# Performance work log

Hardware: AMD Instinct MI355X
Metric: run time of the kernel (lower is better)

## Reference

```python
import jax, jax.numpy as jnp
import numpy as np

B, C, H, W = 32, 3, 512, 512
OUT = (64, 64)  # (out_grid[0]=Nx, out_grid[1]=Ny)
SMALL = 1e-4


def setup_inputs() -> dict:
    key = jax.random.key(0)
    k1, k2 = jax.random.split(key, 2)
    X = jax.random.normal(k1, (B, C, H, W), dtype=jnp.float32)
    fan_in = C * H * W
    # localization net: flatten + dense(5); scaled so p ~ N(0,1) and exp(p) is stable
    W_loc = jax.random.normal(k2, (fan_in, 5), dtype=jnp.float32) / np.float32(np.sqrt(fan_in))
    b_loc = jnp.zeros((5,), dtype=jnp.float32)
    return {"X": X, "W_loc": W_loc, "b_loc": b_loc}


def reference(X, W_loc, b_loc):
    Bn = X.shape[0]
    # locnet: p = flatten(X) @ W_loc + b_loc  -> [B, 5]
    p = X.reshape(Bn, -1) @ W_loc + b_loc

    N = min(OUT)
    gx = OUT[0] * (p[:, 0] + 1.0) / 2.0          # [B]
    gy = OUT[1] * (p[:, 1] + 1.0) / 2.0          # [B]
    sigma2 = jnp.exp(p[:, 2])                    # [B]
    delta = jnp.exp(p[:, 3]) * (max(W, H) - 1) / (N - 1.0)  # [B]
    gamma = jnp.exp(p[:, 4])                     # [B]

    i1 = jnp.arange(OUT[0], dtype=jnp.float32)   # [Nx]
    i2 = jnp.arange(OUT[1], dtype=jnp.float32)   # [Ny]
    a = jnp.arange(W, dtype=jnp.float32)         # [W]
    b = jnp.arange(H, dtype=jnp.float32)         # [H]

    mx = gx[:, None] + delta[:, None] * (i1 - N / 2.0 - 0.5)  # [B, Nx]
    my = gy[:, None] + delta[:, None] * (i2 - N / 2.0 - 0.5)  # [B, Ny]

    Fx = jnp.exp(-((a - mx[:, :, None]) ** 2) / (2.0 * sigma2[:, None, None]))  # [B,Nx,W]
    Fx = Fx / (Fx.sum(axis=-1, keepdims=True) + SMALL)
    Fy = jnp.exp(-((b - my[:, :, None]) ** 2) / (2.0 * sigma2[:, None, None]))  # [B,Ny,H]
    Fy = Fy / (Fy.sum(axis=-1, keepdims=True) + SMALL)

    # glimpse read: gamma * Fy @ X @ Fx^T, done as batched contractions
    Fyx = jnp.einsum('bnh,bchw->bcnw', Fy, X)        # [B,C,Ny,W]
    out = jnp.einsum('bcnw,bmw->bcnm', Fyx, Fx)      # [B,C,Ny,Nx]
    return gamma[:, None, None, None] * out
```

## Files before the change

kernel.cpp:

```cpp
#include <hip/hip_runtime.h>
#include <math.h>

#define B_ 32
#define C_ 3
#define H_ 512
#define W_ 512
#define NOUT 64
#define FAN (C_*H_*W_)

#define CHUNKS 192
#define CELEMS (FAN / CHUNKS)
#define BGROUPS 4

#define PPART_STRIDE 160
#define GAMMA_OFF (CHUNKS * PPART_STRIDE)
#define PFLOATS 32768
#define FXH_U 0
#define FXL_U 1048576
#define FYH_U 2097152
#define FYL_U 3145728

typedef __bf16 bf16x8 __attribute__((ext_vector_type(8)));
typedef float f32x4 __attribute__((ext_vector_type(4)));

__device__ __forceinline__ unsigned short f2bf(float f) {
    unsigned int u = __float_as_uint(f);
    u = (u + 0x7FFFu + ((u >> 16) & 1u)) >> 16;
    return (unsigned short)u;
}
__device__ __forceinline__ float bf2f(unsigned short h) {
    return __uint_as_float(((unsigned int)h) << 16);
}
__device__ __forceinline__ unsigned int cvt_pk_bf16(float lo, float hi) {
    unsigned int r;
    asm("v_cvt_pk_bf16_f32 %0, %1, %2" : "=v"(r) : "v"(lo), "v"(hi));
    return r;
}

__global__ __launch_bounds__(256) void k_locnet(const float* __restrict__ X,
                                                const float* __restrict__ Wl,
                                                float* __restrict__ ws) {
    const int chunk = blockIdx.x;
    const int b0 = blockIdx.y * 8;
    const int t = threadIdx.x;

    float acc[8][5] = {};
    const size_t base = (size_t)chunk * CELEMS;

    for (int k = t; k < CELEMS / 4; k += 256) {
        const size_t i0 = base + (size_t)k * 4;
        const float4* W4 = (const float4*)(Wl + i0 * 5);
        float4 w0 = W4[0], w1 = W4[1], w2 = W4[2], w3 = W4[3], w4 = W4[4];
        float wv[20] = {w0.x, w0.y, w0.z, w0.w,
                        w1.x, w1.y, w1.z, w1.w,
                        w2.x, w2.y, w2.z, w2.w,
                        w3.x, w3.y, w3.z, w3.w,
                        w4.x, w4.y, w4.z, w4.w};
        #pragma unroll
        for (int bb = 0; bb < 8; bb++) {
            float4 x = *(const float4*)(X + (size_t)(b0 + bb) * FAN + i0);
            float xv[4] = {x.x, x.y, x.z, x.w};
            #pragma unroll
            for (int e = 0; e < 4; e++)
                #pragma unroll
                for (int j = 0; j < 5; j++)
                    acc[bb][j] += xv[e] * wv[e * 5 + j];
        }
    }

    #pragma unroll
    for (int off = 32; off > 0; off >>= 1)
        #pragma unroll
        for (int bb = 0; bb < 8; bb++)
            #pragma unroll
            for (int j = 0; j < 5; j++)
                acc[bb][j] += __shfl_down(acc[bb][j], off);

    __shared__ float sred[4][40];
    const int wave = t >> 6, lane = t & 63;
    if (lane == 0) {
        #pragma unroll
        for (int bb = 0; bb < 8; bb++)
            #pragma unroll
            for (int j = 0; j < 5; j++)
                sred[wave][bb * 5 + j] = acc[bb][j];
    }
    __syncthreads();
    if (t < 40) {
        float s = sred[0][t] + sred[1][t] + sred[2][t] + sred[3][t];
        ws[(size_t)chunk * PPART_STRIDE + b0 * 5 + t] = s;
    }
}

__global__ __launch_bounds__(256) void k_filters(const float* __restrict__ bl,
                                                 float* __restrict__ ws,
                                                 float* __restrict__ out) {
    const int n = blockIdx.x;
    const int b = blockIdx.y;
    const int which = blockIdx.z;
    const int t = threadIdx.x;

    {
        const int bid = blockIdx.x + NOUT * (blockIdx.y + B_ * blockIdx.z);
        if (t < 24) {
            ((float4*)out)[(size_t)bid * 24 + t] = make_float4(0.f, 0.f, 0.f, 0.f);
        }
    }

    float pj[5] = {0.f, 0.f, 0.f, 0.f, 0.f};
    if (t < CHUNKS) {
        const float* pr = ws + (size_t)t * PPART_STRIDE + b * 5;
        #pragma unroll
        for (int j = 0; j < 5; j++) pj[j] = pr[j];
    }
    #pragma unroll
    for (int off = 32; off > 0; off >>= 1)
        #pragma unroll
        for (int j = 0; j < 5; j++) pj[j] += __shfl_down(pj[j], off);

    __shared__ float spart[4][5];
    __shared__ float pfin[5];
    const int wave = t >> 6, lane = t & 63;
    if (lane == 0) {
        #pragma unroll
        for (int j = 0; j < 5; j++) spart[wave][j] = pj[j];
    }
    __syncthreads();
    if (t < 5) pfin[t] = spart[0][t] + spart[1][t] + spart[2][t] + spart[3][t] + bl[t];
    __syncthreads();

    const float p0 = pfin[0], p1 = pfin[1], p2 = pfin[2], p3 = pfin[3];
    if (which == 0 && n == 0 && t == 0) ws[GAMMA_OFF + b] = expf(pfin[4]);

    const float g = (which == 0) ? 32.f * (p0 + 1.f) : 32.f * (p1 + 1.f);
    const float sigma2 = expf(p2);
    const float inv2s = 0.5f / sigma2;
    const float delta = expf(p3) * (511.0f / 63.0f);
    const float mean = g + delta * ((float)n - 32.5f);

    float d0 = (float)(2 * t) - mean;
    float f0 = expf(-d0 * d0 * inv2s);
    float d1 = (float)(2 * t + 1) - mean;
    float f1 = expf(-d1 * d1 * inv2s);

    float s = f0 + f1;
    #pragma unroll
    for (int off = 32; off > 0; off >>= 1) s += __shfl_down(s, off);
    __shared__ float sred[4];
    __shared__ float stot;
    if (lane == 0) sred[wave] = s;
    __syncthreads();
    if (t == 0) stot = sred[0] + sred[1] + sred[2] + sred[3] + 1e-4f;
    __syncthreads();
    const float scale = 1.0f / stot;

    unsigned short* wsu = (unsigned short*)(ws + PFLOATS);
    unsigned int* dstH = (unsigned int*)(wsu + (which ? FYH_U : FXH_U) + ((size_t)b * NOUT + n) * 512);
    unsigned int* dstL = (unsigned int*)(wsu + (which ? FYL_U : FXL_U) + ((size_t)b * NOUT + n) * 512);

    float v0 = f0 * scale;
    float v1 = f1 * scale;
    unsigned short h0 = f2bf(v0);
    unsigned short h1 = f2bf(v1);
    unsigned short l0 = f2bf(v0 - bf2f(h0));
    unsigned short l1 = f2bf(v1 - bf2f(h1));
    dstH[t] = (unsigned int)h0 | ((unsigned int)h1 << 16);
    dstL[t] = (unsigned int)l0 | ((unsigned int)l1 << 16);
}

#define KC 64
#define PITCH 72
#define TSZ (64 * PITCH)

#define LOAD_X(wt_) do {                                                      \
    const int wbase_ = (wt_) * KC;                                            \
    _Pragma("unroll")                                                         \
    for (int k4 = 0; k4 < 4; k4++) {                                          \
        int idx_ = t + 256 * k4;                                              \
        int row_ = idx_ >> 4;                                                 \
        int c4_ = (idx_ & 15) * 4;                                            \
        xr[k4] = *(const float4*)(Xp + (size_t)row_ * W_ + wbase_ + c4_);     \
    } } while (0)

#define LOAD_F(Hp_, Lp_, coff_) do {                                          \
    _Pragma("unroll")                                                         \
    for (int i_ = 0; i_ < 2; i_++) {                                          \
        int idx_ = t + 256 * i_;                                              \
        int row_ = idx_ >> 3;                                                 \
        int c8_ = (idx_ & 7) * 8;                                             \
        fhr[i_] = *(const uint4*)((Hp_) + (size_t)row_ * 512 + (coff_) + c8_);\
        flr[i_] = *(const uint4*)((Lp_) + (size_t)row_ * 512 + (coff_) + c8_);\
    } } while (0)

__global__ __launch_bounds__(256) void k_glimpse(const float* __restrict__ X,
                                                 const float* __restrict__ ws,
                                                 float* __restrict__ out) {
    const int hc = blockIdx.x;
    const int bc = blockIdx.y;
    const int b = bc / 3;
    const int t = threadIdx.x;
    const int lane = t & 63;
    const int wv = t >> 6;
    const int l15 = lane & 15;
    const int quad = lane >> 4;
    const int hbase = hc * 64;

    __shared__ __align__(16) unsigned short lds[4 * TSZ];
    unsigned short* Xh = lds;
    unsigned short* Xl = lds + TSZ;
    unsigned short* Fh = lds + 2 * TSZ;
    unsigned short* Fl = lds + 3 * TSZ;

    const float* Xp = X + (size_t)bc * (H_ * W_) + (size_t)hbase * W_;
    const unsigned short* wsu = (const unsigned short*)(ws + PFLOATS);
    const unsigned short* FxHp = wsu + FXH_U + (size_t)b * NOUT * 512;
    const unsigned short* FxLp = wsu + FXL_U + (size_t)b * NOUT * 512;
    const unsigned short* FyHp = wsu + FYH_U + (size_t)b * NOUT * 512;
    const unsigned short* FyLp = wsu + FYL_U + (size_t)b * NOUT * 512;

    float4 xr[4];
    uint4 fhr[2], flr[2];
    LOAD_X(0);
    LOAD_F(FxHp, FxLp, 0);

    f32x4 acc[4] = {};

    for (int wt = 0; wt < 8; wt++) {
        #pragma unroll
        for (int k4 = 0; k4 < 4; k4++) {
            int idx = t + 256 * k4;
            int row = idx >> 4;
            int c4 = (idx & 15) * 4;
            float4 v = xr[k4];
            unsigned int h01 = cvt_pk_bf16(v.x, v.y);
            unsigned int h23 = cvt_pk_bf16(v.z, v.w);
            float r0 = __uint_as_float(h01 << 16);
            float r1 = __uint_as_float(h01 & 0xffff0000u);
            float r2 = __uint_as_float(h23 << 16);
            float r3 = __uint_as_float(h23 & 0xffff0000u);
            unsigned int l01 = cvt_pk_bf16(v.x - r0, v.y - r1);
            unsigned int l23 = cvt_pk_bf16(v.z - r2, v.w - r3);
            int o = row * PITCH + c4;
            *(uint2*)&Xh[o] = make_uint2(h01, h23);
            *(uint2*)&Xl[o] = make_uint2(l01, l23);
        }
        #pragma unroll
        for (int i = 0; i < 2; i++) {
            int idx = t + 256 * i;
            int row = idx >> 3;
            int c8 = (idx & 7) * 8;
            *(uint4*)&Fh[row * PITCH + c8] = fhr[i];
            *(uint4*)&Fl[row * PITCH + c8] = flr[i];
        }
        __syncthreads();

        if (wt < 7) {
            LOAD_X(wt + 1);
            LOAD_F(FxHp, FxLp, (wt + 1) * KC);
        } else {
            LOAD_F(FyHp, FyLp, hbase);
        }

        #pragma unroll
        for (int ks = 0; ks < 2; ks++) {
            const int ko = ks * 32 + quad * 8;
            bf16x8 ah = *(const bf16x8*)&Xh[(16 * wv + l15) * PITCH + ko];
            bf16x8 al = *(const bf16x8*)&Xl[(16 * wv + l15) * PITCH + ko];
            #pragma unroll
            for (int mt = 0; mt < 4; mt++) {
                bf16x8 bh = *(const bf16x8*)&Fh[(16 * mt + l15) * PITCH + ko];
                bf16x8 bl2 = *(const bf16x8*)&Fl[(16 * mt + l15) * PITCH + ko];
                acc[mt] = __builtin_amdgcn_mfma_f32_16x16x32_bf16(ah, bh, acc[mt], 0, 0, 0);
                acc[mt] = __builtin_amdgcn_mfma_f32_16x16x32_bf16(al, bh, acc[mt], 0, 0, 0);
                acc[mt] = __builtin_amdgcn_mfma_f32_16x16x32_bf16(ah, bl2, acc[mt], 0, 0, 0);
            }
        }
        __syncthreads();
    }

    #pragma unroll
    for (int mt = 0; mt < 4; mt++) {
        float g0 = acc[mt][0], g1 = acc[mt][1], g2 = acc[mt][2], g3 = acc[mt][3];
        unsigned int h01 = cvt_pk_bf16(g0, g1);
        unsigned int h23 = cvt_pk_bf16(g2, g3);
        float r0 = __uint_as_float(h01 << 16);
        float r1 = __uint_as_float(h01 & 0xffff0000u);
        float r2 = __uint_as_float(h23 << 16);
        float r3 = __uint_as_float(h23 & 0xffff0000u);
        unsigned int l01 = cvt_pk_bf16(g0 - r0, g1 - r1);
        unsigned int l23 = cvt_pk_bf16(g2 - r2, g3 - r3);
        int m = 16 * mt + l15;
        int h = 16 * wv + quad * 4;
        int o = m * PITCH + h;
        *(uint2*)&Xh[o] = make_uint2(h01, h23);
        *(uint2*)&Xl[o] = make_uint2(l01, l23);
    }

    #pragma unroll
    for (int i = 0; i < 2; i++) {
        int idx = t + 256 * i;
        int row = idx >> 3;
        int c8 = (idx & 7) * 8;
        *(uint4*)&Fh[row * PITCH + c8] = fhr[i];
        *(uint4*)&Fl[row * PITCH + c8] = flr[i];
    }
    __syncthreads();

    f32x4 p[4] = {};
    #pragma unroll
    for (int ks = 0; ks < 2; ks++) {
        const int ko = ks * 32 + quad * 8;
        bf16x8 yh = *(const bf16x8*)&Fh[(16 * wv + l15) * PITCH + ko];
        bf16x8 yl = *(const bf16x8*)&Fl[(16 * wv + l15) * PITCH + ko];
        #pragma unroll
        for (int mt = 0; mt < 4; mt++) {
            bf16x8 gh = *(const bf16x8*)&Xh[(16 * mt + l15) * PITCH + ko];
            bf16x8 gl = *(const bf16x8*)&Xl[(16 * mt + l15) * PITCH + ko];
            p[mt] = __builtin_amdgcn_mfma_f32_16x16x32_bf16(yh, gh, p[mt], 0, 0, 0);
            p[mt] = __builtin_amdgcn_mfma_f32_16x16x32_bf16(yl, gh, p[mt], 0, 0, 0);
            p[mt] = __builtin_amdgcn_mfma_f32_16x16x32_bf16(yh, gl, p[mt], 0, 0, 0);
        }
    }

    const float gamma = ws[GAMMA_OFF + b];
    float* outp = out + (size_t)bc * (NOUT * NOUT);
    #pragma unroll
    for (int mt = 0; mt < 4; mt++)
        #pragma unroll
        for (int r = 0; r < 4; r++) {
            int n = 16 * wv + quad * 4 + r;
            int m = 16 * mt + l15;
            atomicAdd(&outp[n * NOUT + m], gamma * p[mt][r]);
        }
}

extern "C" void kernel_launch(void* const* d_in, const int* in_sizes, int n_in,
                              void* d_out, int out_size, void* d_ws, size_t ws_size,
                              hipStream_t stream) {
    const float* X  = (const float*)d_in[0];
    const float* Wl = (const float*)d_in[1];
    const float* bl = (const float*)d_in[2];
    float* out = (float*)d_out;
    float* ws  = (float*)d_ws;

    k_locnet<<<dim3(CHUNKS, BGROUPS), 256, 0, stream>>>(X, Wl, ws);
    k_filters<<<dim3(NOUT, B_, 2), 256, 0, stream>>>(bl, ws, out);
    k_glimpse<<<dim3(8, B_ * C_), 256, 0, stream>>>(X, ws, out);
}
```

Before: 222.1 us.

## Feed X straight from global into MFMA registers and double-buffer Fx in LDS

The glimpse kernel no longer stages X through shared memory. Each lane loads its own 8-float row slice of X from global, splits it into bf16 hi/lo in registers, and passes it directly as the MFMA A operand. The Fx tiles are ping-ponged between two LDS buffers (reusing the old X buffers), so each iteration needs one barrier instead of two. The intent is to cut LDS traffic and barriers. The cost is that X loads are issued just before use, with a less coalesced pattern, and the Fy tile load is no longer prefetched before the second GEMM.

```diff
diff --git a/kernel.cpp b/kernel.cpp
--- a/kernel.cpp
+++ b/kernel.cpp
@@ -36,6 +36,8 @@
     asm("v_cvt_pk_bf16_f32 %0, %1, %2" : "=v"(r) : "v"(lo), "v"(hi));
     return r;
 }
+
+union BF8U { uint4 u; bf16x8 v; };
 
 __global__ __launch_bounds__(256) void k_locnet(const float* __restrict__ X,
                                                 const float* __restrict__ Wl,
@@ -171,26 +173,6 @@
 #define KC 64
 #define PITCH 72
 #define TSZ (64 * PITCH)
-
-#define LOAD_X(wt_) do {                                                      \
-    const int wbase_ = (wt_) * KC;                                            \
-    _Pragma("unroll")                                                         \
-    for (int k4 = 0; k4 < 4; k4++) {                                          \
-        int idx_ = t + 256 * k4;                                              \
-        int row_ = idx_ >> 4;                                                 \
-        int c4_ = (idx_ & 15) * 4;                                            \
-        xr[k4] = *(const float4*)(Xp + (size_t)row_ * W_ + wbase_ + c4_);     \
-    } } while (0)
-
-#define LOAD_F(Hp_, Lp_, coff_) do {                                          \
-    _Pragma("unroll")                                                         \
-    for (int i_ = 0; i_ < 2; i_++) {                                          \
-        int idx_ = t + 256 * i_;                                              \
-        int row_ = idx_ >> 3;                                                 \
-        int c8_ = (idx_ & 7) * 8;                                             \
-        fhr[i_] = *(const uint4*)((Hp_) + (size_t)row_ * 512 + (coff_) + c8_);\
-        flr[i_] = *(const uint4*)((Lp_) + (size_t)row_ * 512 + (coff_) + c8_);\
-    } } while (0)
 
 __global__ __launch_bounds__(256) void k_glimpse(const float* __restrict__ X,
                                                  const float* __restrict__ ws,
@@ -218,62 +200,76 @@
     const unsigned short* FyHp = wsu + FYH_U + (size_t)b * NOUT * 512;
     const unsigned short* FyLp = wsu + FYL_U + (size_t)b * NOUT * 512;
 
-    float4 xr[4];
-    uint4 fhr[2], flr[2];
-    LOAD_X(0);
-    LOAD_F(FxHp, FxLp, 0);
+    const float* xlane = Xp + (size_t)(16 * wv + l15) * W_ + quad * 8;
+
+    const int srow0 = t >> 3;
+    const int sc8 = (t & 7) * 8;
+
+    {
+        uint4 h0 = *(const uint4*)(FxHp + (size_t)srow0 * 512 + sc8);
+        uint4 l0 = *(const uint4*)(FxLp + (size_t)srow0 * 512 + sc8);
+        uint4 h1 = *(const uint4*)(FxHp + (size_t)(srow0 + 32) * 512 + sc8);
+        uint4 l1 = *(const uint4*)(FxLp + (size_t)(srow0 + 32) * 512 + sc8);
+        *(uint4*)&Fh[srow0 * PITCH + sc8] = h0;
+        *(uint4*)&Fl[srow0 * PITCH + sc8] = l0;
+        *(uint4*)&Fh[(srow0 + 32) * PITCH + sc8] = h1;
+        *(uint4*)&Fl[(srow0 + 32) * PITCH + sc8] = l1;
+    }
+    __syncthreads();
 
     f32x4 acc[4] = {};
 
+    #pragma unroll
     for (int wt = 0; wt < 8; wt++) {
-        #pragma unroll
-        for (int k4 = 0; k4 < 4; k4++) {
-            int idx = t + 256 * k4;
-            int row = idx >> 4;
-            int c4 = (idx & 15) * 4;
-            float4 v = xr[k4];
-            unsigned int h01 = cvt_pk_bf16(v.x, v.y);
-            unsigned int h23 = cvt_pk_bf16(v.z, v.w);
-            float r0 = __uint_as_float(h01 << 16);
-            float r1 = __uint_as_float(h01 & 0xffff0000u);
-            float r2 = __uint_as_float(h23 << 16);
-            float r3 = __uint_as_float(h23 & 0xffff0000u);
-            unsigned int l01 = cvt_pk_bf16(v.x - r0, v.y - r1);
-            unsigned int l23 = cvt_pk_bf16(v.z - r2, v.w - r3);
-            int o = row * PITCH + c4;
-            *(uint2*)&Xh[o] = make_uint2(h01, h23);
-            *(uint2*)&Xl[o] = make_uint2(l01, l23);
-        }
-        #pragma unroll
-        for (int i = 0; i < 2; i++) {
-            int idx = t + 256 * i;
-            int row = idx >> 3;
-            int c8 = (idx & 7) * 8;
-            *(uint4*)&Fh[row * PITCH + c8] = fhr[i];
-            *(uint4*)&Fl[row * PITCH + c8] = flr[i];
-        }
-        __syncthreads();
-
+        unsigned short* curH = (wt & 1) ? Xh : Fh;
+        unsigned short* curL = (wt & 1) ? Xl : Fl;
+        unsigned short* nxtH = (wt & 1) ? Fh : Xh;
+        unsigned short* nxtL = (wt & 1) ? Fl : Xl;
+
+        uint4 nh0, nl0, nh1, nl1;
         if (wt < 7) {
-            LOAD_X(wt + 1);
-            LOAD_F(FxHp, FxLp, (wt + 1) * KC);
-        } else {
-            LOAD_F(FyHp, FyLp, hbase);
+            const int wb = (wt + 1) * KC;
+            nh0 = *(const uint4*)(FxHp + (size_t)srow0 * 512 + wb + sc8);
+            nl0 = *(const uint4*)(FxLp + (size_t)srow0 * 512 + wb + sc8);
+            nh1 = *(const uint4*)(FxHp + (size_t)(srow0 + 32) * 512 + wb + sc8);
+            nl1 = *(const uint4*)(FxLp + (size_t)(srow0 + 32) * 512 + wb + sc8);
         }
 
         #pragma unroll
         for (int ks = 0; ks < 2; ks++) {
+            const float* xp = xlane + wt * KC + ks * 32;
+            float4 x0 = *(const float4*)(xp);
+            float4 x1 = *(const float4*)(xp + 4);
+            BF8U ah, al;
+            ah.u.x = cvt_pk_bf16(x0.x, x0.y);
+            ah.u.y = cvt_pk_bf16(x0.z, x0.w);
+            ah.u.z = cvt_pk_bf16(x1.x, x1.y);
+            ah.u.w = cvt_pk_bf16(x1.z, x1.w);
+            al.u.x = cvt_pk_bf16(x0.x - __uint_as_float(ah.u.x << 16),
+                                 x0.y - __uint_as_float(ah.u.x & 0xffff0000u));
+            al.u.y = cvt_pk_bf16(x0.z - __uint_as_float(ah.u.y << 16),
+                                 x0.w - __uint_as_float(ah.u.y & 0xffff0000u));
+            al.u.z = cvt_pk_bf16(x1.x - __uint_as_float(ah.u.z << 16),
+                                 x1.y - __uint_as_float(ah.u.z & 0xffff0000u));
+            al.u.w = cvt_pk_bf16(x1.z - __uint_as_float(ah.u.w << 16),
+                                 x1.w - __uint_as_float(ah.u.w & 0xffff0000u));
+
             const int ko = ks * 32 + quad * 8;
-            bf16x8 ah = *(const bf16x8*)&Xh[(16 * wv + l15) * PITCH + ko];
-            bf16x8 al = *(const bf16x8*)&Xl[(16 * wv + l15) * PITCH + ko];
             #pragma unroll
             for (int mt = 0; mt < 4; mt++) {
-                bf16x8 bh = *(const bf16x8*)&Fh[(16 * mt + l15) * PITCH + ko];
-                bf16x8 bl2 = *(const bf16x8*)&Fl[(16 * mt + l15) * PITCH + ko];
-                acc[mt] = __builtin_amdgcn_mfma_f32_16x16x32_bf16(ah, bh, acc[mt], 0, 0, 0);
-                acc[mt] = __builtin_amdgcn_mfma_f32_16x16x32_bf16(al, bh, acc[mt], 0, 0, 0);
-                acc[mt] = __builtin_amdgcn_mfma_f32_16x16x32_bf16(ah, bl2, acc[mt], 0, 0, 0);
+                bf16x8 bh = *(const bf16x8*)&curH[(16 * mt + l15) * PITCH + ko];
+                bf16x8 bl2 = *(const bf16x8*)&curL[(16 * mt + l15) * PITCH + ko];
+                acc[mt] = __builtin_amdgcn_mfma_f32_16x16x32_bf16(ah.v, bh, acc[mt], 0, 0, 0);
+                acc[mt] = __builtin_amdgcn_mfma_f32_16x16x32_bf16(al.v, bh, acc[mt], 0, 0, 0);
+                acc[mt] = __builtin_amdgcn_mfma_f32_16x16x32_bf16(ah.v, bl2, acc[mt], 0, 0, 0);
             }
+        }
+
+        if (wt < 7) {
+            *(uint4*)&nxtH[srow0 * PITCH + sc8] = nh0;
+            *(uint4*)&nxtL[srow0 * PITCH + sc8] = nl0;
+            *(uint4*)&nxtH[(srow0 + 32) * PITCH + sc8] = nh1;
+            *(uint4*)&nxtL[(srow0 + 32) * PITCH + sc8] = nl1;
         }
         __syncthreads();
     }
@@ -296,13 +292,15 @@
         *(uint2*)&Xl[o] = make_uint2(l01, l23);
     }
 
-    #pragma unroll
-    for (int i = 0; i < 2; i++) {
-        int idx = t + 256 * i;
-        int row = idx >> 3;
-        int c8 = (idx & 7) * 8;
-        *(uint4*)&Fh[row * PITCH + c8] = fhr[i];
-        *(uint4*)&Fl[row * PITCH + c8] = flr[i];
+    {
+        uint4 h0 = *(const uint4*)(FyHp + (size_t)srow0 * 512 + hbase + sc8);
+        uint4 l0 = *(const uint4*)(FyLp + (size_t)srow0 * 512 + hbase + sc8);
+        uint4 h1 = *(const uint4*)(FyHp + (size_t)(srow0 + 32) * 512 + hbase + sc8);
+        uint4 l1 = *(const uint4*)(FyLp + (size_t)(srow0 + 32) * 512 + hbase + sc8);
+        *(uint4*)&Fh[srow0 * PITCH + sc8] = h0;
+        *(uint4*)&Fl[srow0 * PITCH + sc8] = l0;
+        *(uint4*)&Fh[(srow0 + 32) * PITCH + sc8] = h1;
+        *(uint4*)&Fl[(srow0 + 32) * PITCH + sc8] = l1;
     }
     __syncthreads();
 
```

Result: faster. 203.2 us (median of 2 runs) (-8.5%).
